# Performance work log

Measured on AMD Instinct MI355X. Metric: run time of the kernel, lower is better.

Reference implementation:

```python
import jax, jax.numpy as jnp
import numpy as np

NUM_HEADS = 12


def setup_inputs() -> dict:
    key = jax.random.key(0)
    ks = jax.random.split(key, 5)
    B, N, C = 4, 2048, 768
    s = 0.02
    return {
        "x": jax.random.normal(ks[0], (B, N, C), jnp.float32),
        "qkv_w": jax.random.normal(ks[1], (3 * C, C), jnp.float32) * s,
        "qkv_b": jax.random.normal(ks[2], (3 * C,), jnp.float32) * s,
        "proj_w": jax.random.normal(ks[3], (C, C), jnp.float32) * s,
        "proj_b": jax.random.normal(ks[4], (C,), jnp.float32) * s,
    }


def reference(x, qkv_w, qkv_b, proj_w, proj_b):
    B, N, C = x.shape
    H = NUM_HEADS
    D = C // H
    scale = D ** -0.5
    # qkv projection: [B,N,3C] -> [3,B,H,N,D]
    qkv = (x @ qkv_w.T + qkv_b).reshape(B, N, 3, H, D).transpose(2, 0, 3, 1, 4)
    q, k, v = qkv[0], qkv[1], qkv[2]
    attn = jnp.einsum("bhnd,bhmd->bhnm", q, k) * scale  # [B,H,N,N]
    attn_probs = jax.nn.softmax(attn, axis=-1)
    # dropout p=0 (eval) -> identity
    out = jnp.einsum("bhnm,bhmd->bhnd", attn_probs, v)  # [B,H,N,D]
    out = out.transpose(0, 2, 1, 3).reshape(B, N, C)
    return out @ proj_w.T + proj_b
```

## Files before the change

kernel.cpp:

```cpp
#include <hip/hip_runtime.h>

typedef __attribute__((ext_vector_type(8))) short bf16x8;
typedef __attribute__((ext_vector_type(4))) float f32x4;
typedef __attribute__((ext_vector_type(4))) unsigned int u32x4;

#define QSCALE 0.1803368801111243f

__device__ inline unsigned short f2bf(float f) {
  union { float f; unsigned u; } v; v.f = f;
  unsigned r = v.u + 0x7fffu + ((v.u >> 16) & 1u);
  return (unsigned short)(r >> 16);
}

__device__ inline unsigned packbf2(float a, float b) {
  union { float f; unsigned u; } va, vb; va.f = a; vb.f = b;
  unsigned ta = va.u + 0x7fffu + ((va.u >> 16) & 1u);
  unsigned tb = vb.u + 0x7fffu + ((vb.u >> 16) & 1u);
  return __builtin_amdgcn_perm(tb, ta, 0x07060302);
}

__device__ inline void async16(const void* g, void* l) {
  __builtin_amdgcn_global_load_lds(
      (const __attribute__((address_space(1))) unsigned int*)g,
      (__attribute__((address_space(3))) unsigned int*)l, 16, 0, 0);
}


__device__ inline void swz_one(const float* __restrict__ src, unsigned short* __restrict__ dst,
                               int idx) {
  int l16 = idx & 15, quad = (idx >> 4) & 3, mi = (idx >> 6) & 3;
  int rest = idx >> 8;
  int cg = rest % 24, g = rest / 24;
  int row = g * 64 + mi * 16 + l16;
  int k = cg * 32 + quad * 8;
  const float* s = src + (size_t)row * 768 + k;
  float4 v0 = *(const float4*)s, v1 = *(const float4*)(s + 4);
  u32x4 o;
  o.x = packbf2(v0.x, v0.y); o.y = packbf2(v0.z, v0.w);
  o.z = packbf2(v1.x, v1.y); o.w = packbf2(v1.z, v1.w);
  *(u32x4*)(dst + (size_t)idx * 8) = o;
}

__global__ __launch_bounds__(256) void swz_x(const float* __restrict__ x,
                                             unsigned short* __restrict__ xs) {
  swz_one(x, xs, blockIdx.x * 256 + threadIdx.x);
}

__global__ __launch_bounds__(256) void swz_w(const float* __restrict__ wq,
                                             const float* __restrict__ wp,
                                             unsigned short* __restrict__ wqs,
                                             unsigned short* __restrict__ wps) {
  int idx = blockIdx.x * 256 + threadIdx.x;
  if (idx < 221184) swz_one(wq, wqs, idx);
  else              swz_one(wp, wps, idx - 221184);
}

template<int MODE>
__global__ __launch_bounds__(256, MODE == 0 ? 3 : 4) void gemm_swz(
    const unsigned short* __restrict__ A, const unsigned short* __restrict__ B,
    const float* __restrict__ bias,
    unsigned short* __restrict__ oq, unsigned short* __restrict__ ok,
    unsigned short* __restrict__ ov, float* __restrict__ of)
{
  constexpr int NI = (MODE == 0) ? 4 : 2;
  const int t = threadIdx.x, w = t >> 6, lane = t & 63;
  const int quad = lane >> 4, l16 = lane & 15;
  const int bm = blockIdx.x, bn = blockIdx.y;

  const int gA = (MODE == 0) ? (bm * 2 + (w >> 1)) : bm;
  const unsigned short* Ab = A + (size_t)gA * 49152 + (size_t)lane * 8;

  const unsigned short* Bb[NI];
#pragma unroll
  for (int ni = 0; ni < NI; ni++) {
    int n_base = bn * 128 + ((MODE == 0) ? (w & 1) * 64 : w * 32) + ni * 16;
    Bb[ni] = B + (size_t)(n_base >> 6) * 49152 + (size_t)((n_base >> 4) & 3) * 512
               + (size_t)lane * 8;
  }

  f32x4 acc[4][NI] = {};
  bf16x8 af[2][4], bf_[2][NI];

#pragma unroll
  for (int mi = 0; mi < 4; mi++) af[0][mi] = *(const bf16x8*)(Ab + mi * 512);
#pragma unroll
  for (int ni = 0; ni < NI; ni++) bf_[0][ni] = *(const bf16x8*)(Bb[ni]);

#pragma unroll
  for (int cg = 0; cg < 24; cg++) {
    const int cur = cg & 1;
    if (cg < 23) {
#pragma unroll
      for (int mi = 0; mi < 4; mi++)
        af[cur ^ 1][mi] = *(const bf16x8*)(Ab + (cg + 1) * 2048 + mi * 512);
#pragma unroll
      for (int ni = 0; ni < NI; ni++)
        bf_[cur ^ 1][ni] = *(const bf16x8*)(Bb[ni] + (cg + 1) * 2048);
    }
#pragma unroll
    for (int mi = 0; mi < 4; mi++)
#pragma unroll
      for (int ni = 0; ni < NI; ni++)
        acc[mi][ni] = __builtin_amdgcn_mfma_f32_16x16x32_bf16(af[cur][mi], bf_[cur][ni],
                                                              acc[mi][ni], 0, 0, 0);
  }

  if (MODE == 0) {
    const int three = (bn * 128) / 768;
#pragma unroll
    for (int ni = 0; ni < NI; ni++) {
      int n_g = bn * 128 + (w & 1) * 64 + ni * 16 + l16;
      float bs = bias[n_g];
      int rem = n_g - three * 768;
      int h = rem >> 6, d = rem & 63;
#pragma unroll
      for (int mi = 0; mi < 4; mi++) {
#pragma unroll
        for (int r = 0; r < 4; r++) {
          int m_g = gA * 64 + mi * 16 + (quad << 2) + r;
          int b_ = m_g >> 11, ntok = m_g & 2047;
          float v = acc[mi][ni][r] + bs;
          if (three == 0)
            oq[(((size_t)b_ * 12 + h) * 2048 + ntok) * 64 + d] = f2bf(v * QSCALE);
          else if (three == 1)
            ok[(((size_t)b_ * 12 + h) * 2048 + ntok) * 64 + d] = f2bf(v);
          else
            ov[(((size_t)b_ * 12 + h) * 64 + d) * 2048 + ntok] = f2bf(v);
        }
      }
    }
  } else {
#pragma unroll
    for (int ni = 0; ni < NI; ni++) {
      int n_g = bn * 128 + w * 32 + ni * 16 + l16;
      float bs = bias[n_g];
#pragma unroll
      for (int mi = 0; mi < 4; mi++) {
#pragma unroll
        for (int r = 0; r < 4; r++) {
          int m_g = bm * 64 + mi * 16 + (quad << 2) + r;
          of[(size_t)m_g * 768 + n_g] = acc[mi][ni][r] + bs;
        }
      }
    }
  }
}

__global__ __launch_bounds__(256, 3) void flash_attn(
    const unsigned short* __restrict__ Qb, const unsigned short* __restrict__ Kb,
    const unsigned short* __restrict__ Vtb, unsigned short* __restrict__ aos)
{
  __shared__ unsigned short Ks[2][4096];
  __shared__ unsigned short Vs[2][4096];
  const int t = threadIdx.x, w = t >> 6, lane = t & 63;
  const int quad = lane >> 4, l16 = lane & 15;
  const int bh = blockIdx.x, qt = blockIdx.y;
  const unsigned short* Qg = Qb + (size_t)bh * 2048 * 64;
  const unsigned short* Kg = Kb + (size_t)bh * 2048 * 64;
  const unsigned short* Vg = Vtb + (size_t)bh * 2048 * 64;

  bf16x8 bq[2][2];
#pragma unroll
  for (int u = 0; u < 2; u++) {
    int qrow = qt * 128 + w * 32 + u * 16 + l16;
#pragma unroll
    for (int h = 0; h < 2; h++)
      bq[u][h] = *(const bf16x8*)(Qg + (size_t)qrow * 64 + h * 32 + quad * 8);
  }

  const int s0 = t, s1 = 256 + t;
  auto gperm = [](int s) { return (s & 0x23) | ((s & 0x0c) << 1) | ((s & 0x10) >> 2); };
  const size_t koff0 = (size_t)gperm(s0 & 63) * 64 + (s0 >> 6) * 8;
  const size_t koff1 = (size_t)gperm(s1 & 63) * 64 + (s1 >> 6) * 8;
  const size_t voff0 = (size_t)(s0 & 63) * 2048 + (s0 >> 6) * 8;
  const size_t voff1 = (size_t)(s1 & 63) * 2048 + (s1 >> 6) * 8;

  float l_run[2] = {0.f, 0.f};
  f32x4 o_acc[2][4];
#pragma unroll
  for (int u = 0; u < 2; u++)
#pragma unroll
    for (int dt = 0; dt < 4; dt++) o_acc[u][dt] = (f32x4){0.f, 0.f, 0.f, 0.f};

  async16(Kg + koff0, &Ks[0][s0 * 8]);
  async16(Kg + koff1, &Ks[0][s1 * 8]);
  async16(Vg + voff0, &Vs[0][s0 * 8]);
  async16(Vg + voff1, &Vs[0][s1 * 8]);

  for (int kt = 0; kt < 32; kt++) {
    const int p = kt & 1;
    __syncthreads();
    if (kt < 31) {
      const unsigned short* Kn = Kg + (size_t)(kt + 1) * 4096;
      const unsigned short* Vn = Vg + (size_t)(kt + 1) * 64;
      async16(Kn + koff0, &Ks[p ^ 1][s0 * 8]);
      async16(Kn + koff1, &Ks[p ^ 1][s1 * 8]);
      async16(Vn + voff0, &Vs[p ^ 1][s0 * 8]);
      async16(Vn + voff1, &Vs[p ^ 1][s1 * 8]);
    }
    const unsigned short* Kp = &Ks[p][0];
    const unsigned short* Vp = &Vs[p][0];

    f32x4 sv[2][4];
#pragma unroll
    for (int nt = 0; nt < 4; nt++) {
      bf16x8 k0 = *(const bf16x8*)&Kp[((quad) * 64 + nt * 16 + l16) * 8];
      bf16x8 k1 = *(const bf16x8*)&Kp[((4 + quad) * 64 + nt * 16 + l16) * 8];
#pragma unroll
      for (int u = 0; u < 2; u++) {
        f32x4 s_ = {0.f, 0.f, 0.f, 0.f};
        s_ = __builtin_amdgcn_mfma_f32_16x16x32_bf16(k0, bq[u][0], s_, 0, 0, 0);
        s_ = __builtin_amdgcn_mfma_f32_16x16x32_bf16(k1, bq[u][1], s_, 0, 0, 0);
        sv[u][nt] = s_;
      }
    }

    union { unsigned u32[8]; bf16x8 v[2]; } pk[2];
#pragma unroll
    for (int u = 0; u < 2; u++) {
#pragma unroll
      for (int nt = 0; nt < 4; nt++) {
        float p0 = __builtin_amdgcn_exp2f(sv[u][nt][0]);
        float p1 = __builtin_amdgcn_exp2f(sv[u][nt][1]);
        float p2 = __builtin_amdgcn_exp2f(sv[u][nt][2]);
        float p3 = __builtin_amdgcn_exp2f(sv[u][nt][3]);
        l_run[u] += (p0 + p1) + (p2 + p3);
        pk[u].u32[nt * 2]     = packbf2(p0, p1);
        pk[u].u32[nt * 2 + 1] = packbf2(p2, p3);
      }
    }

#pragma unroll
    for (int cc = 0; cc < 2; cc++) {
#pragma unroll
      for (int dt = 0; dt < 4; dt++) {
        bf16x8 a = *(const bf16x8*)&Vp[((cc * 4 + quad) * 64 + dt * 16 + l16) * 8];
#pragma unroll
        for (int u = 0; u < 2; u++)
          o_acc[u][dt] = __builtin_amdgcn_mfma_f32_16x16x32_bf16(a, pk[u].v[cc], o_acc[u][dt], 0, 0, 0);
      }
    }
  }

  float linv[2];
#pragma unroll
  for (int u = 0; u < 2; u++) {
    float l = l_run[u];
    l += __shfl_xor(l, 16, 64);
    l += __shfl_xor(l, 32, 64);
    linv[u] = 1.f / l;
  }

  const int b_ = bh / 12, h = bh - b_ * 12;
  const int g_ = b_ * 32 + qt * 2 + (w >> 1);
#pragma unroll
  for (int u = 0; u < 2; u++) {
    const int mi = (w * 2 + u) & 3;
    unsigned short* base = aos + (size_t)g_ * 49152 + mi * 512 + l16 * 8;
#pragma unroll
    for (int dt = 0; dt < 4; dt++) {
      int cg = h * 2 + (dt >> 1);
      int cq = (dt & 1) * 2 + (quad >> 1);
#pragma unroll
      for (int pr = 0; pr < 2; pr++) {
        float v0 = o_acc[u][dt][pr * 2] * linv[u];
        float v1 = o_acc[u][dt][pr * 2 + 1] * linv[u];
        int j = (quad & 1) * 4 + pr * 2;
        *(unsigned*)(base + cg * 2048 + cq * 128 + j) = packbf2(v0, v1);
      }
    }
  }
}

extern "C" void kernel_launch(void* const* d_in, const int* in_sizes, int n_in,
                              void* d_out, int out_size, void* d_ws, size_t ws_size,
                              hipStream_t stream) {
  const float* x      = (const float*)d_in[0];
  const float* qkv_w  = (const float*)d_in[1];
  const float* qkv_b  = (const float*)d_in[2];
  const float* proj_w = (const float*)d_in[3];
  const float* proj_b = (const float*)d_in[4];
  float* out = (float*)d_out;

  unsigned short* ws  = (unsigned short*)d_ws;
  unsigned short* wqs = ws;
  unsigned short* wps = wqs + 1769472;
  unsigned short* xs  = wps + 589824;
  unsigned short* qb  = xs + 6291456;
  unsigned short* kb  = qb + 6291456;
  unsigned short* vtb = kb + 6291456;
  unsigned short* aos = vtb + 6291456;

  swz_w<<<1152, 256, 0, stream>>>(qkv_w, proj_w, wqs, wps);
  swz_x<<<3072, 256, 0, stream>>>(x, xs);
  gemm_swz<0><<<dim3(64, 18), 256, 0, stream>>>(xs, wqs, qkv_b, qb, kb, vtb, nullptr);
  flash_attn<<<dim3(48, 16), 256, 0, stream>>>(qb, kb, vtb, aos);
  gemm_swz<1><<<dim3(128, 6), 256, 0, stream>>>(aos, wps, proj_b, nullptr, nullptr, nullptr, out);
}
```

Before: 238.0 us.

## Replace pre-swizzled direct-load GEMMs with LDS-staged row-major GEMMs

Drops the swizzled blocked layout for x, weights and attention output and keeps plain row-major bf16 casts. Both GEMMs now stage 128xTN tiles in shared memory through async global-to-LDS loads with an XOR swizzle, so A/B fragments are reused across warps instead of each warp loading straight from global memory. The epilogues and the flash-attention output write vectorized packed stores, including a u32x2 store for the transposed V. The price is two barriers per k-step with no double buffering, which may expose load latency, and the proj GEMM grid changes to 64x12 with a lower occupancy hint.

```diff
diff --git a/kernel.cpp b/kernel.cpp
--- a/kernel.cpp
+++ b/kernel.cpp
@@ -3,6 +3,7 @@
 typedef __attribute__((ext_vector_type(8))) short bf16x8;
 typedef __attribute__((ext_vector_type(4))) float f32x4;
 typedef __attribute__((ext_vector_type(4))) unsigned int u32x4;
+typedef __attribute__((ext_vector_type(2))) unsigned int u32x2;
 
 #define QSCALE 0.1803368801111243f
 
@@ -25,130 +26,162 @@
       (__attribute__((address_space(3))) unsigned int*)l, 16, 0, 0);
 }
 
-
-__device__ inline void swz_one(const float* __restrict__ src, unsigned short* __restrict__ dst,
-                               int idx) {
-  int l16 = idx & 15, quad = (idx >> 4) & 3, mi = (idx >> 6) & 3;
-  int rest = idx >> 8;
-  int cg = rest % 24, g = rest / 24;
-  int row = g * 64 + mi * 16 + l16;
-  int k = cg * 32 + quad * 8;
-  const float* s = src + (size_t)row * 768 + k;
+__device__ inline void cast8(const float* __restrict__ s, unsigned short* __restrict__ d) {
   float4 v0 = *(const float4*)s, v1 = *(const float4*)(s + 4);
   u32x4 o;
   o.x = packbf2(v0.x, v0.y); o.y = packbf2(v0.z, v0.w);
   o.z = packbf2(v1.x, v1.y); o.w = packbf2(v1.z, v1.w);
-  *(u32x4*)(dst + (size_t)idx * 8) = o;
-}
-
-__global__ __launch_bounds__(256) void swz_x(const float* __restrict__ x,
-                                             unsigned short* __restrict__ xs) {
-  swz_one(x, xs, blockIdx.x * 256 + threadIdx.x);
-}
-
-__global__ __launch_bounds__(256) void swz_w(const float* __restrict__ wq,
-                                             const float* __restrict__ wp,
-                                             unsigned short* __restrict__ wqs,
-                                             unsigned short* __restrict__ wps) {
+  *(u32x4*)d = o;
+}
+
+__global__ __launch_bounds__(256) void cast_x(const float* __restrict__ x,
+                                              unsigned short* __restrict__ xs) {
+  size_t idx = (size_t)blockIdx.x * 256 + threadIdx.x;
+  cast8(x + idx * 8, xs + idx * 8);
+}
+
+__global__ __launch_bounds__(256) void cast_w(const float* __restrict__ wq,
+                                              const float* __restrict__ wp,
+                                              unsigned short* __restrict__ wqs,
+                                              unsigned short* __restrict__ wps) {
   int idx = blockIdx.x * 256 + threadIdx.x;
-  if (idx < 221184) swz_one(wq, wqs, idx);
-  else              swz_one(wp, wps, idx - 221184);
+  if (idx < 221184) cast8(wq + (size_t)idx * 8, wqs + (size_t)idx * 8);
+  else {
+    size_t j = (size_t)(idx - 221184) * 8;
+    cast8(wp + j, wps + j);
+  }
 }
 
 template<int MODE>
-__global__ __launch_bounds__(256, MODE == 0 ? 3 : 4) void gemm_swz(
+__global__ __launch_bounds__(256, 3) void gemm_lds(
     const unsigned short* __restrict__ A, const unsigned short* __restrict__ B,
     const float* __restrict__ bias,
     unsigned short* __restrict__ oq, unsigned short* __restrict__ ok,
     unsigned short* __restrict__ ov, float* __restrict__ of)
 {
   constexpr int NI = (MODE == 0) ? 4 : 2;
+  constexpr int TN = NI * 32;
+  __shared__ unsigned short As[128 * 64];
+  __shared__ unsigned short Bs[TN * 64];
+
   const int t = threadIdx.x, w = t >> 6, lane = t & 63;
   const int quad = lane >> 4, l16 = lane & 15;
   const int bm = blockIdx.x, bn = blockIdx.y;
-
-  const int gA = (MODE == 0) ? (bm * 2 + (w >> 1)) : bm;
-  const unsigned short* Ab = A + (size_t)gA * 49152 + (size_t)lane * 8;
-
-  const unsigned short* Bb[NI];
-#pragma unroll
-  for (int ni = 0; ni < NI; ni++) {
-    int n_base = bn * 128 + ((MODE == 0) ? (w & 1) * 64 : w * 32) + ni * 16;
-    Bb[ni] = B + (size_t)(n_base >> 6) * 49152 + (size_t)((n_base >> 4) & 3) * 512
-               + (size_t)lane * 8;
+  const int wr = w >> 1, wc = w & 1;
+
+  const int r_off = lane >> 3;
+  const int kb_lin = (lane & 7) << 4;
+
+  const unsigned short* Ag = A + (size_t)(bm * 128) * 768;
+  const unsigned short* Bg = B + (size_t)(bn * TN) * 768;
+
+  const unsigned short* ApA[4]; unsigned short* LpA[4];
+#pragma unroll
+  for (int i = 0; i < 4; i++) {
+    int r = w * 32 + i * 8 + r_off;
+    int ks = (kb_lin ^ ((r & 7) << 4)) >> 1;
+    ApA[i] = Ag + (size_t)r * 768 + ks;
+    LpA[i] = As + (w * 32 + i * 8) * 64 + lane * 8;
+  }
+  const unsigned short* ApB[NI]; unsigned short* LpB[NI];
+#pragma unroll
+  for (int i = 0; i < NI; i++) {
+    int r = w * (TN / 4) + i * 8 + r_off;
+    int ks = (kb_lin ^ ((r & 7) << 4)) >> 1;
+    ApB[i] = Bg + (size_t)r * 768 + ks;
+    LpB[i] = Bs + (w * (TN / 4) + i * 8) * 64 + lane * 8;
   }
 
   f32x4 acc[4][NI] = {};
-  bf16x8 af[2][4], bf_[2][NI];
-
-#pragma unroll
-  for (int mi = 0; mi < 4; mi++) af[0][mi] = *(const bf16x8*)(Ab + mi * 512);
-#pragma unroll
-  for (int ni = 0; ni < NI; ni++) bf_[0][ni] = *(const bf16x8*)(Bb[ni]);
-
-#pragma unroll
-  for (int cg = 0; cg < 24; cg++) {
-    const int cur = cg & 1;
-    if (cg < 23) {
+  const int swz = (l16 & 7) << 3;
+
+  for (int kt = 0; kt < 12; kt++) {
+    __syncthreads();
+    const int k0 = kt * 64;
+#pragma unroll
+    for (int i = 0; i < 4; i++)  async16(ApA[i] + k0, LpA[i]);
+#pragma unroll
+    for (int i = 0; i < NI; i++) async16(ApB[i] + k0, LpB[i]);
+    __syncthreads();
+
+#pragma unroll
+    for (int kc = 0; kc < 2; kc++) {
+      const int ko = (kc * 32 + quad * 8) ^ swz;
+      bf16x8 a[4], b[NI];
 #pragma unroll
       for (int mi = 0; mi < 4; mi++)
-        af[cur ^ 1][mi] = *(const bf16x8*)(Ab + (cg + 1) * 2048 + mi * 512);
+        a[mi] = *(const bf16x8*)&As[(wr * 64 + mi * 16 + l16) * 64 + ko];
 #pragma unroll
       for (int ni = 0; ni < NI; ni++)
-        bf_[cur ^ 1][ni] = *(const bf16x8*)(Bb[ni] + (cg + 1) * 2048);
-    }
-#pragma unroll
-    for (int mi = 0; mi < 4; mi++)
+        b[ni] = *(const bf16x8*)&Bs[(wc * (TN / 2) + ni * 16 + l16) * 64 + ko];
+#pragma unroll
+      for (int mi = 0; mi < 4; mi++)
+#pragma unroll
+        for (int ni = 0; ni < NI; ni++)
+          acc[mi][ni] = __builtin_amdgcn_mfma_f32_16x16x32_bf16(a[mi], b[ni],
+                                                                acc[mi][ni], 0, 0, 0);
+    }
+  }
+
+  const int m_base = bm * 128 + wr * 64;
+  if (MODE == 0) {
+    const int three = (bn * TN) / 768;
+    int hh[NI], dd[NI]; float bb[NI];
+#pragma unroll
+    for (int ni = 0; ni < NI; ni++) {
+      int n_g = bn * TN + wc * (TN / 2) + ni * 16 + l16;
+      bb[ni] = bias[n_g];
+      int rem = n_g - three * 768;
+      hh[ni] = rem >> 6; dd[ni] = rem & 63;
+    }
+    if (three == 2) {
 #pragma unroll
       for (int ni = 0; ni < NI; ni++)
-        acc[mi][ni] = __builtin_amdgcn_mfma_f32_16x16x32_bf16(af[cur][mi], bf_[cur][ni],
-                                                              acc[mi][ni], 0, 0, 0);
-  }
-
-  if (MODE == 0) {
-    const int three = (bn * 128) / 768;
+#pragma unroll
+        for (int mi = 0; mi < 4; mi++) {
+          int m0 = m_base + mi * 16 + (quad << 2);
+          int b_ = m0 >> 11, ntok = m0 & 2047;
+          u32x2 pv;
+          pv.x = packbf2(acc[mi][ni][0] + bb[ni], acc[mi][ni][1] + bb[ni]);
+          pv.y = packbf2(acc[mi][ni][2] + bb[ni], acc[mi][ni][3] + bb[ni]);
+          *(u32x2*)(ov + (((size_t)b_ * 12 + hh[ni]) * 64 + dd[ni]) * 2048 + ntok) = pv;
+        }
+    } else {
+      unsigned short* o = (three == 0) ? oq : ok;
+      const float sc = (three == 0) ? QSCALE : 1.f;
+#pragma unroll
+      for (int mi = 0; mi < 4; mi++)
+#pragma unroll
+        for (int r = 0; r < 4; r++) {
+          int m_g = m_base + mi * 16 + (quad << 2) + r;
+          int b_ = m_g >> 11, ntok = m_g & 2047;
+          size_t rowb = ((size_t)b_ * 12) * 2048;
+#pragma unroll
+          for (int ni = 0; ni < NI; ni++) {
+            float v = (acc[mi][ni][r] + bb[ni]) * sc;
+            o[((rowb + (size_t)hh[ni] * 2048 + ntok) << 6) + dd[ni]] = f2bf(v);
+          }
+        }
+    }
+  } else {
 #pragma unroll
     for (int ni = 0; ni < NI; ni++) {
-      int n_g = bn * 128 + (w & 1) * 64 + ni * 16 + l16;
+      int n_g = bn * TN + wc * (TN / 2) + ni * 16 + l16;
       float bs = bias[n_g];
-      int rem = n_g - three * 768;
-      int h = rem >> 6, d = rem & 63;
-#pragma unroll
-      for (int mi = 0; mi < 4; mi++) {
+#pragma unroll
+      for (int mi = 0; mi < 4; mi++)
 #pragma unroll
         for (int r = 0; r < 4; r++) {
-          int m_g = gA * 64 + mi * 16 + (quad << 2) + r;
-          int b_ = m_g >> 11, ntok = m_g & 2047;
-          float v = acc[mi][ni][r] + bs;
-          if (three == 0)
-            oq[(((size_t)b_ * 12 + h) * 2048 + ntok) * 64 + d] = f2bf(v * QSCALE);
-          else if (three == 1)
-            ok[(((size_t)b_ * 12 + h) * 2048 + ntok) * 64 + d] = f2bf(v);
-          else
-            ov[(((size_t)b_ * 12 + h) * 64 + d) * 2048 + ntok] = f2bf(v);
-        }
-      }
-    }
-  } else {
-#pragma unroll
-    for (int ni = 0; ni < NI; ni++) {
-      int n_g = bn * 128 + w * 32 + ni * 16 + l16;
-      float bs = bias[n_g];
-#pragma unroll
-      for (int mi = 0; mi < 4; mi++) {
-#pragma unroll
-        for (int r = 0; r < 4; r++) {
-          int m_g = bm * 64 + mi * 16 + (quad << 2) + r;
+          int m_g = m_base + mi * 16 + (quad << 2) + r;
           of[(size_t)m_g * 768 + n_g] = acc[mi][ni][r] + bs;
         }
-      }
     }
   }
 }
 
 __global__ __launch_bounds__(256, 3) void flash_attn(
     const unsigned short* __restrict__ Qb, const unsigned short* __restrict__ Kb,
-    const unsigned short* __restrict__ Vtb, unsigned short* __restrict__ aos)
+    const unsigned short* __restrict__ Vtb, unsigned short* __restrict__ ao)
 {
   __shared__ unsigned short Ks[2][4096];
   __shared__ unsigned short Vs[2][4096];
@@ -252,22 +285,16 @@
   }
 
   const int b_ = bh / 12, h = bh - b_ * 12;
-  const int g_ = b_ * 32 + qt * 2 + (w >> 1);
 #pragma unroll
   for (int u = 0; u < 2; u++) {
-    const int mi = (w * 2 + u) & 3;
-    unsigned short* base = aos + (size_t)g_ * 49152 + mi * 512 + l16 * 8;
+    int row = b_ * 2048 + qt * 128 + w * 32 + u * 16 + l16;
+    unsigned short* base = ao + (size_t)row * 768 + h * 64 + (quad << 2);
 #pragma unroll
     for (int dt = 0; dt < 4; dt++) {
-      int cg = h * 2 + (dt >> 1);
-      int cq = (dt & 1) * 2 + (quad >> 1);
-#pragma unroll
-      for (int pr = 0; pr < 2; pr++) {
-        float v0 = o_acc[u][dt][pr * 2] * linv[u];
-        float v1 = o_acc[u][dt][pr * 2 + 1] * linv[u];
-        int j = (quad & 1) * 4 + pr * 2;
-        *(unsigned*)(base + cg * 2048 + cq * 128 + j) = packbf2(v0, v1);
-      }
+      u32x2 pv;
+      pv.x = packbf2(o_acc[u][dt][0] * linv[u], o_acc[u][dt][1] * linv[u]);
+      pv.y = packbf2(o_acc[u][dt][2] * linv[u], o_acc[u][dt][3] * linv[u]);
+      *(u32x2*)(base + dt * 16) = pv;
     }
   }
 }
@@ -289,11 +316,11 @@
   unsigned short* qb  = xs + 6291456;
   unsigned short* kb  = qb + 6291456;
   unsigned short* vtb = kb + 6291456;
-  unsigned short* aos = vtb + 6291456;
-
-  swz_w<<<1152, 256, 0, stream>>>(qkv_w, proj_w, wqs, wps);
-  swz_x<<<3072, 256, 0, stream>>>(x, xs);
-  gemm_swz<0><<<dim3(64, 18), 256, 0, stream>>>(xs, wqs, qkv_b, qb, kb, vtb, nullptr);
-  flash_attn<<<dim3(48, 16), 256, 0, stream>>>(qb, kb, vtb, aos);
-  gemm_swz<1><<<dim3(128, 6), 256, 0, stream>>>(aos, wps, proj_b, nullptr, nullptr, nullptr, out);
-}
+  unsigned short* ao  = vtb + 6291456;
+
+  cast_w<<<1152, 256, 0, stream>>>(qkv_w, proj_w, wqs, wps);
+  cast_x<<<3072, 256, 0, stream>>>(x, xs);
+  gemm_lds<0><<<dim3(64, 18), 256, 0, stream>>>(xs, wqs, qkv_b, qb, kb, vtb, nullptr);
+  flash_attn<<<dim3(48, 16), 256, 0, stream>>>(qb, kb, vtb, ao);
+  gemm_lds<1><<<dim3(64, 12), 256, 0, stream>>>(ao, wps, proj_b, nullptr, nullptr, nullptr, out);
+}
```

Result: faster. 212.2 us (-10.9%).
